# Performance work log

Hardware: AMD Instinct MI355X
Metric: run time of the kernel (lower is better)

The kernel has to match this reference:

```python
import jax, jax.numpy as jnp
import numpy as np

N_ACTOR = 128
NUM_MODS = 6
NUM_PTS = 30
N = 32768
B = 64
EPS = 1e-5


def _gn(x, g, b):
    # torch GroupNorm(1, C) on [..., C]: normalize over channel axis, affine
    m = jnp.mean(x, axis=-1, keepdims=True)
    v = jnp.mean((x - m) ** 2, axis=-1, keepdims=True)
    return (x - m) * jax.lax.rsqrt(v + EPS) * g + b


def setup_inputs() -> dict:
    key = jax.random.key(0)
    ks = jax.random.split(key, 32)
    d = N_ACTOR
    M = NUM_MODS
    s = 0.05
    rn = lambda k, shp: jax.random.normal(k, shp, jnp.float32) * s
    inp = {
        'actors': jax.random.normal(ks[0], (N, d), jnp.float32),
        'actor_ctrs': jax.random.normal(ks[1], (N, 2), jnp.float32),
        'actor_idcs': jnp.arange(N, dtype=jnp.int32).reshape(B, N // B),
        # per-mode residual MLP + output linear (stacked over modes)
        'pred_W1': rn(ks[2], (M, d, d)),
        'pred_g1': jnp.ones((M, d), jnp.float32),
        'pred_b1': jnp.zeros((M, d), jnp.float32),
        'pred_W2': rn(ks[3], (M, d, d)),
        'pred_g2': jnp.ones((M, d), jnp.float32),
        'pred_b2': jnp.zeros((M, d), jnp.float32),
        'pred_Wo': rn(ks[4], (M, d, 2 * NUM_PTS)),
        'pred_bo': rn(ks[5], (M, 2 * NUM_PTS)),
        # cls head: residual MLP + Linear(d,1)
        'cls_W1': rn(ks[6], (d, d)),
        'cls_g1': jnp.ones((d,), jnp.float32),
        'cls_b1': jnp.zeros((d,), jnp.float32),
        'cls_W2': rn(ks[7], (d, d)),
        'cls_g2': jnp.ones((d,), jnp.float32),
        'cls_b2': jnp.zeros((d,), jnp.float32),
        'cls_Wo': rn(ks[8], (d, 1)),
        'cls_bo': rn(ks[9], (1,)),
        # AttDest
        'att_dW1': rn(ks[10], (2, d)),
        'att_db1': rn(ks[11], (d,)),
        'att_dW2': rn(ks[12], (d, d)),
        'att_dg2': jnp.ones((d,), jnp.float32),
        'att_db2': jnp.zeros((d,), jnp.float32),
        'att_aW': rn(ks[13], (2 * d, d)),
        'att_ag': jnp.ones((d,), jnp.float32),
        'att_ab': jnp.zeros((d,), jnp.float32),
    }
    return inp


def reference(actors, actor_ctrs, actor_idcs, pred_W1, pred_g1, pred_b1,
              pred_W2, pred_g2, pred_b2, pred_Wo, pred_bo,
              cls_W1, cls_g1, cls_b1, cls_W2, cls_g2, cls_b2, cls_Wo, cls_bo,
              att_dW1, att_db1, att_dW2, att_dg2, att_db2,
              att_aW, att_ag, att_ab):
    n = actors.shape[0]
    M = pred_W1.shape[0]
    h = jnp.einsum('nc,mcd->mnd', actors, pred_W1)              # [M,N,d]
    h = jax.nn.relu(_gn(h, pred_g1[:, None, :], pred_b1[:, None, :]))
    h = _gn(jnp.einsum('mnd,mde->mne', h, pred_W2),
            pred_g2[:, None, :], pred_b2[:, None, :])
    h = jax.nn.relu(h + actors[None])                           # residual
    preds = jnp.einsum('mnd,mdo->mno', h, pred_Wo) + pred_bo[:, None, :]
    reg = preds.transpose(1, 0, 2).reshape(n, M, NUM_PTS, 2)    # [N,M,T,2]
    # per-scene reg[idcs] += ctrs: actor_idcs partitions arange(N), so this
    # is exactly a per-actor broadcast add of the (concatenated) centers
    reg = reg + actor_ctrs[:, None, None, :]
    dest_ctrs = jax.lax.stop_gradient(reg[:, :, -1, :])         # .detach()
    # --- AttDest ---
    dist = (actor_ctrs[:, None, :] - dest_ctrs).reshape(-1, 2)  # [N*M,2]
    dist = jax.nn.relu(dist @ att_dW1 + att_db1)
    dist = jax.nn.relu(_gn(dist @ att_dW2, att_dg2, att_db2))
    agts = jnp.broadcast_to(actors[:, None, :], (n, M, actors.shape[1]))
    agts = agts.reshape(-1, actors.shape[1])
    feats = jax.nn.relu(_gn(jnp.concatenate([dist, agts], axis=1) @ att_aW,
                            att_ag, att_ab))                    # [N*M,d]
    # --- cls head ---
    c = jax.nn.relu(_gn(feats @ cls_W1, cls_g1, cls_b1))
    c = _gn(c @ cls_W2, cls_g2, cls_b2)
    c = jax.nn.relu(c + feats)
    cls = (c @ cls_Wo + cls_bo).reshape(n, M)
    # --- sort modes by descending score, reorder reg accordingly ---
    order = jnp.argsort(-cls, axis=1)
    cls = jnp.take_along_axis(cls, order, axis=1)
    reg = jnp.take_along_axis(reg, order[:, :, None, None], axis=1)
    # train_model=True concatenates the per-scene splits back in order,
    # which reproduces the full arrays
    return cls, reg
```

## Files before the change

kernel.cpp:

```cpp
#include <hip/hip_runtime.h>

#define EPSV 1e-5f
#define CLS_SZ (32768*6)

#define AL(ch,row) (((ch)<<7) + ((row) ^ ((((ch)&15))<<3)))

__device__ __forceinline__ float4 ld4(const float* p) { return *reinterpret_cast<const float4*>(p); }
__device__ __forceinline__ void st4(float* p, float4 v) { *reinterpret_cast<float4*>(p) = v; }

__device__ __forceinline__ void gemmA(const float* X, const float* __restrict__ Wg,
                                      float* WB0, float* WB1, float (&acc)[8][8],
                                      int ag, int jg4, int tid)
{
  float4 rA = ld4(Wg + tid*4);
  float4 rB = ld4(Wg + 1024 + tid*4);
  __syncthreads();
  st4(WB0 + tid*4, rA);
  st4(WB1 + tid*4, rB);
  __syncthreads();
  #pragma unroll 1
  for (int c = 0; c < 16; ++c) {
    float4 rN;
    const bool pf = (c + 2 < 16);
    if (pf) rN = ld4(Wg + (c+2)*1024 + tid*4);
    const float* WB = (c & 1) ? WB1 : WB0;
    #pragma unroll
    for (int kk = 0; kk < 8; ++kk) {
      int k = c*8 + kk;
      const float* xp = X + (k<<7) + ((ag<<3) ^ ((k & 15)<<3));
      float4 x0 = ld4(xp), x1 = ld4(xp + 4);
      float4 wl = ld4(WB + (kk<<7) + jg4);
      float4 wh = ld4(WB + (kk<<7) + 64 + jg4);
      float xv[8] = {x0.x,x0.y,x0.z,x0.w,x1.x,x1.y,x1.z,x1.w};
      float wv[8] = {wl.x,wl.y,wl.z,wl.w,wh.x,wh.y,wh.z,wh.w};
      #pragma unroll
      for (int r = 0; r < 8; ++r)
        #pragma unroll
        for (int c2 = 0; c2 < 8; ++c2)
          acc[r][c2] = fmaf(xv[r], wv[c2], acc[r][c2]);
    }
    __syncthreads();
    if (pf) st4(((c & 1) ? WB1 : WB0) + tid*4, rN);
  }
}

__device__ __forceinline__ void gemmWo(const float* X, const float* __restrict__ Wg,
                                       float* WB0, float* WB1, float (&acc)[8][4],
                                       int ag, int jg, int tid)
{
  const bool ld = tid < 120;
  const bool zp = (tid >= 120 && tid < 128);
  const int kk0 = ld ? (tid / 15) : (tid - 120);
  const int sl  = ld ? (tid % 15) * 4 : 60;
  float4 rA = {0,0,0,0}, rB = {0,0,0,0};
  if (ld) { rA = ld4(Wg + kk0*60 + sl); rB = ld4(Wg + 480 + kk0*60 + sl); }
  __syncthreads();
  if (ld || zp) { st4(WB0 + (kk0<<6) + sl, rA); st4(WB1 + (kk0<<6) + sl, rB); }
  __syncthreads();
  #pragma unroll 1
  for (int c = 0; c < 16; ++c) {
    float4 rN = {0,0,0,0};
    const bool pf = (c + 2 < 16);
    if (pf && ld) rN = ld4(Wg + (c+2)*480 + kk0*60 + sl);
    const float* WB = (c & 1) ? WB1 : WB0;
    #pragma unroll
    for (int kk = 0; kk < 8; ++kk) {
      int k = c*8 + kk;
      const float* xp = X + (k<<7) + ((ag<<3) ^ ((k & 15)<<3));
      float4 x0 = ld4(xp), x1 = ld4(xp + 4);
      float4 w = ld4(WB + (kk<<6) + jg*4);
      float xv[8] = {x0.x,x0.y,x0.z,x0.w,x1.x,x1.y,x1.z,x1.w};
      float wv[4] = {w.x,w.y,w.z,w.w};
      #pragma unroll
      for (int r = 0; r < 8; ++r)
        #pragma unroll
        for (int c2 = 0; c2 < 4; ++c2)
          acc[r][c2] = fmaf(xv[r], wv[c2], acc[r][c2]);
    }
    __syncthreads();
    if (pf && (ld || zp)) st4(((c & 1) ? WB1 : WB0) + (kk0<<6) + sl, rN);
  }
}

__device__ __forceinline__ void gn_finish(float* PS1, float* PS2, float* MEAN, float* RSTD, int tid)
{
  __syncthreads();
  if (tid < 128) {
    float a = 0.f, b = 0.f;
    #pragma unroll
    for (int j = 0; j < 4; ++j) { a += PS1[tid*4 + j]; b += PS2[tid*4 + j]; }
    float mu = a * 0.0078125f;
    float var = b * 0.0078125f - mu*mu;
    MEAN[tid] = mu;
    RSTD[tid] = rsqrtf(var + EPSV);
  }
  __syncthreads();
}

__device__ __forceinline__ void gn_reduce8(const float (&acc)[8][8], float* PS1, float* PS2,
                                           float* MEAN, float* RSTD, int ag, int jg, int tid)
{
  #pragma unroll
  for (int r = 0; r < 8; ++r) {
    float s = 0.f, q = 0.f;
    #pragma unroll
    for (int c = 0; c < 8; ++c) { float v = acc[r][c]; s += v; q += v*v; }
    s += __shfl_xor(s, 1, 64); q += __shfl_xor(q, 1, 64);
    s += __shfl_xor(s, 2, 64); q += __shfl_xor(q, 2, 64);
    if ((jg & 3) == 0) { int row = ag*8 + r; PS1[row*4 + (jg>>2)] = s; PS2[row*4 + (jg>>2)] = q; }
  }
  gn_finish(PS1, PS2, MEAN, RSTD, tid);
}

__global__ void __launch_bounds__(256, 2) pred_kernel(
    const float* __restrict__ actors, const float* __restrict__ ctrs,
    const float* __restrict__ W1, const float* __restrict__ g1v, const float* __restrict__ b1v,
    const float* __restrict__ W2, const float* __restrict__ g2v, const float* __restrict__ b2v,
    const float* __restrict__ Wo, const float* __restrict__ bov,
    float* __restrict__ out_reg)
{
  __shared__ __align__(16) float ACT[16384];
  __shared__ __align__(16) float WB0[1024], WB1[1024];
  __shared__ float MEAN[128], RSTD[128];
  float* PS1 = WB0;
  float* PS2 = WB1;

  const int tid = threadIdx.x;
  const int jg = tid & 15, ag = tid >> 4;
  const int jg4 = jg*4;
  const int m  = blockIdx.y;
  const int n0 = blockIdx.x * 128;

  #pragma unroll
  for (int p = 0; p < 16; ++p) {
    int i = (p<<8) + tid;
    int r = i >> 5, q4 = (i & 31) << 2;
    float4 v = ld4(actors + (size_t)(n0 + r)*128 + q4);
    ACT[AL(q4+0, r)] = v.x; ACT[AL(q4+1, r)] = v.y;
    ACT[AL(q4+2, r)] = v.z; ACT[AL(q4+3, r)] = v.w;
  }

  float acc[8][8];
  #pragma unroll
  for (int r = 0; r < 8; ++r)
    #pragma unroll
    for (int c = 0; c < 8; ++c) acc[r][c] = 0.f;

  gemmA(ACT, W1 + (size_t)m*16384, WB0, WB1, acc, ag, jg4, tid);
  gn_reduce8(acc, PS1, PS2, MEAN, RSTD, ag, jg, tid);
  {
    float mu[8], rs[8];
    #pragma unroll
    for (int r = 0; r < 8; ++r) { mu[r] = MEAN[ag*8+r]; rs[r] = RSTD[ag*8+r]; }
    float4 gl = ld4(g1v + m*128 + jg4), gh = ld4(g1v + m*128 + 64 + jg4);
    float4 bl = ld4(b1v + m*128 + jg4), bh = ld4(b1v + m*128 + 64 + jg4);
    float gv[8] = {gl.x,gl.y,gl.z,gl.w,gh.x,gh.y,gh.z,gh.w};
    float bv[8] = {bl.x,bl.y,bl.z,bl.w,bh.x,bh.y,bh.z,bh.w};
    float vm[8][8];
    #pragma unroll
    for (int r = 0; r < 8; ++r)
      #pragma unroll
      for (int c = 0; c < 8; ++c)
        vm[r][c] = fmaxf((acc[r][c] - mu[r]) * rs[r] * gv[c] + bv[c], 0.f);
    #pragma unroll
    for (int c = 0; c < 8; ++c) {
      int ch = (c < 4) ? (jg4 + c) : (64 + jg4 + (c - 4));
      int base = (ch<<7) + ((ag<<3) ^ ((ch & 15)<<3));
      st4(ACT + base,     make_float4(vm[0][c],vm[1][c],vm[2][c],vm[3][c]));
      st4(ACT + base + 4, make_float4(vm[4][c],vm[5][c],vm[6][c],vm[7][c]));
    }
  }

  #pragma unroll
  for (int r = 0; r < 8; ++r)
    #pragma unroll
    for (int c = 0; c < 8; ++c) acc[r][c] = 0.f;

  gemmA(ACT, W2 + (size_t)m*16384, WB0, WB1, acc, ag, jg4, tid);
  gn_reduce8(acc, PS1, PS2, MEAN, RSTD, ag, jg, tid);
  {
    float mu[8], rs[8];
    #pragma unroll
    for (int r = 0; r < 8; ++r) { mu[r] = MEAN[ag*8+r]; rs[r] = RSTD[ag*8+r]; }
    float4 gl = ld4(g2v + m*128 + jg4), gh = ld4(g2v + m*128 + 64 + jg4);
    float4 bl = ld4(b2v + m*128 + jg4), bh = ld4(b2v + m*128 + 64 + jg4);
    float gv[8] = {gl.x,gl.y,gl.z,gl.w,gh.x,gh.y,gh.z,gh.w};
    float bv[8] = {bl.x,bl.y,bl.z,bl.w,bh.x,bh.y,bh.z,bh.w};
    float vm[8][8];
    #pragma unroll
    for (int r = 0; r < 8; ++r) {
      const float* ap = actors + (size_t)(n0 + ag*8 + r)*128;
      float4 a0 = ld4(ap + jg4), a1 = ld4(ap + 64 + jg4);
      float av[8] = {a0.x,a0.y,a0.z,a0.w,a1.x,a1.y,a1.z,a1.w};
      #pragma unroll
      for (int c = 0; c < 8; ++c)
        vm[r][c] = fmaxf((acc[r][c] - mu[r]) * rs[r] * gv[c] + bv[c] + av[c], 0.f);
    }
    #pragma unroll
    for (int c = 0; c < 8; ++c) {
      int ch = (c < 4) ? (jg4 + c) : (64 + jg4 + (c - 4));
      int base = (ch<<7) + ((ag<<3) ^ ((ch & 15)<<3));
      st4(ACT + base,     make_float4(vm[0][c],vm[1][c],vm[2][c],vm[3][c]));
      st4(ACT + base + 4, make_float4(vm[4][c],vm[5][c],vm[6][c],vm[7][c]));
    }
  }

  float acc2[8][4];
  #pragma unroll
  for (int r = 0; r < 8; ++r)
    #pragma unroll
    for (int c = 0; c < 4; ++c) acc2[r][c] = 0.f;
  gemmWo(ACT, Wo + (size_t)m*7680, WB0, WB1, acc2, ag, jg, tid);

  if (jg < 15) {
    float4 bo4 = ld4(bov + m*60 + jg4);
    #pragma unroll
    for (int r = 0; r < 8; ++r) {
      int n = n0 + ag*8 + r;
      float2 cc = *reinterpret_cast<const float2*>(ctrs + 2*n);
      float4 v;
      v.x = acc2[r][0] + bo4.x + cc.x;
      v.y = acc2[r][1] + bo4.y + cc.y;
      v.z = acc2[r][2] + bo4.z + cc.x;
      v.w = acc2[r][3] + bo4.w + cc.y;
      st4(out_reg + (size_t)n*360 + m*60 + jg4, v);
    }
  }
}

__global__ void __launch_bounds__(256, 2) att_cls_kernel(
    const float* __restrict__ actors, const float* __restrict__ ctrs,
    const float* __restrict__ dW1, const float* __restrict__ db1,
    const float* __restrict__ dW2, const float* __restrict__ dg2, const float* __restrict__ db2,
    const float* __restrict__ aW, const float* __restrict__ aG, const float* __restrict__ aB,
    const float* __restrict__ cW1, const float* __restrict__ cg1, const float* __restrict__ cb1,
    const float* __restrict__ cW2, const float* __restrict__ cg2, const float* __restrict__ cb2,
    const float* __restrict__ cWo, const float* __restrict__ cbo,
    const float* __restrict__ reg, float* __restrict__ cls_out)
{
  __shared__ __align__(16) float ACT[16384];
  __shared__ __align__(16) float WB0[1024], WB1[1024];
  __shared__ float MEAN[128], RSTD[128];
  float* PS1 = WB0;
  float* PS2 = WB1;
  float* D0x = MEAN;
  float* D0y = RSTD;

  const int tid = threadIdx.x;
  const int jg = tid & 15, ag = tid >> 4;
  const int jg4 = jg*4;
  const int r0 = blockIdx.x * 128;

  if (tid < 128) {
    int rg = r0 + tid;
    int n = rg / 6, mm = rg - 6*n;
    size_t base = (size_t)n*360 + mm*60;
    float2 c2 = *reinterpret_cast<const float2*>(ctrs + 2*n);
    D0x[tid] = c2.x - reg[base + 58];
    D0y[tid] = c2.y - reg[base + 59];
  }
  __syncthreads();

  {
    float dx[8], dy[8];
    #pragma unroll
    for (int r = 0; r < 8; ++r) { dx[r] = D0x[ag*8+r]; dy[r] = D0y[ag*8+r]; }
    #pragma unroll
    for (int c = 0; c < 8; ++c) {
      int ch = (c < 4) ? (jg4 + c) : (64 + jg4 + (c - 4));
      float w1 = dW1[ch], w2 = dW1[128 + ch], bb = db1[ch];
      float v[8];
      #pragma unroll
      for (int r = 0; r < 8; ++r) v[r] = fmaxf(fmaf(dx[r], w1, fmaf(dy[r], w2, bb)), 0.f);
      int base = (ch<<7) + ((ag<<3) ^ ((ch & 15)<<3));
      st4(ACT + base,     make_float4(v[0],v[1],v[2],v[3]));
      st4(ACT + base + 4, make_float4(v[4],v[5],v[6],v[7]));
    }
  }

  float acc[8][8];
  #pragma unroll
  for (int r = 0; r < 8; ++r)
    #pragma unroll
    for (int c = 0; c < 8; ++c) acc[r][c] = 0.f;

  gemmA(ACT, dW2, WB0, WB1, acc, ag, jg4, tid);
  gn_reduce8(acc, PS1, PS2, MEAN, RSTD, ag, jg, tid);
  {
    float mu[8], rs[8];
    #pragma unroll
    for (int r = 0; r < 8; ++r) { mu[r] = MEAN[ag*8+r]; rs[r] = RSTD[ag*8+r]; }
    float4 gl = ld4(dg2 + jg4), gh = ld4(dg2 + 64 + jg4);
    float4 bl = ld4(db2 + jg4), bh = ld4(db2 + 64 + jg4);
    float gv[8] = {gl.x,gl.y,gl.z,gl.w,gh.x,gh.y,gh.z,gh.w};
    float bv[8] = {bl.x,bl.y,bl.z,bl.w,bh.x,bh.y,bh.z,bh.w};
    float vm[8][8];
    #pragma unroll
    for (int r = 0; r < 8; ++r)
      #pragma unroll
      for (int c = 0; c < 8; ++c)
        vm[r][c] = fmaxf((acc[r][c] - mu[r]) * rs[r] * gv[c] + bv[c], 0.f);
    #pragma unroll
    for (int c = 0; c < 8; ++c) {
      int ch = (c < 4) ? (jg4 + c) : (64 + jg4 + (c - 4));
      int base = (ch<<7) + ((ag<<3) ^ ((ch & 15)<<3));
      st4(ACT + base,     make_float4(vm[0][c],vm[1][c],vm[2][c],vm[3][c]));
      st4(ACT + base + 4, make_float4(vm[4][c],vm[5][c],vm[6][c],vm[7][c]));
    }
  }

  #pragma unroll
  for (int r = 0; r < 8; ++r)
    #pragma unroll
    for (int c = 0; c < 8; ++c) acc[r][c] = 0.f;
  gemmA(ACT, aW, WB0, WB1, acc, ag, jg4, tid);
  #pragma unroll
  for (int p = 0; p < 16; ++p) {
    int i = (p<<8) + tid;
    int r = i >> 5, q4 = (i & 31) << 2;
    int n = (r0 + r) / 6;
    float4 v = ld4(actors + (size_t)n*128 + q4);
    ACT[AL(q4+0, r)] = v.x; ACT[AL(q4+1, r)] = v.y;
    ACT[AL(q4+2, r)] = v.z; ACT[AL(q4+3, r)] = v.w;
  }
  gemmA(ACT, aW + 16384, WB0, WB1, acc, ag, jg4, tid);
  gn_reduce8(acc, PS1, PS2, MEAN, RSTD, ag, jg, tid);
  float feats[8][8];
  {
    float mu[8], rs[8];
    #pragma unroll
    for (int r = 0; r < 8; ++r) { mu[r] = MEAN[ag*8+r]; rs[r] = RSTD[ag*8+r]; }
    float4 gl = ld4(aG + jg4), gh = ld4(aG + 64 + jg4);
    float4 bl = ld4(aB + jg4), bh = ld4(aB + 64 + jg4);
    float gv[8] = {gl.x,gl.y,gl.z,gl.w,gh.x,gh.y,gh.z,gh.w};
    float bv[8] = {bl.x,bl.y,bl.z,bl.w,bh.x,bh.y,bh.z,bh.w};
    #pragma unroll
    for (int r = 0; r < 8; ++r)
      #pragma unroll
      for (int c = 0; c < 8; ++c)
        feats[r][c] = fmaxf((acc[r][c] - mu[r]) * rs[r] * gv[c] + bv[c], 0.f);
    #pragma unroll
    for (int c = 0; c < 8; ++c) {
      int ch = (c < 4) ? (jg4 + c) : (64 + jg4 + (c - 4));
      int base = (ch<<7) + ((ag<<3) ^ ((ch & 15)<<3));
      st4(ACT + base,     make_float4(feats[0][c],feats[1][c],feats[2][c],feats[3][c]));
      st4(ACT + base + 4, make_float4(feats[4][c],feats[5][c],feats[6][c],feats[7][c]));
    }
  }

  #pragma unroll
  for (int r = 0; r < 8; ++r)
    #pragma unroll
    for (int c = 0; c < 8; ++c) acc[r][c] = 0.f;
  gemmA(ACT, cW1, WB0, WB1, acc, ag, jg4, tid);
  gn_reduce8(acc, PS1, PS2, MEAN, RSTD, ag, jg, tid);
  {
    float mu[8], rs[8];
    #pragma unroll
    for (int r = 0; r < 8; ++r) { mu[r] = MEAN[ag*8+r]; rs[r] = RSTD[ag*8+r]; }
    float4 gl = ld4(cg1 + jg4), gh = ld4(cg1 + 64 + jg4);
    float4 bl = ld4(cb1 + jg4), bh = ld4(cb1 + 64 + jg4);
    float gv[8] = {gl.x,gl.y,gl.z,gl.w,gh.x,gh.y,gh.z,gh.w};
    float bv[8] = {bl.x,bl.y,bl.z,bl.w,bh.x,bh.y,bh.z,bh.w};
    float vm[8][8];
    #pragma unroll
    for (int r = 0; r < 8; ++r)
      #pragma unroll
      for (int c = 0; c < 8; ++c)
        vm[r][c] = fmaxf((acc[r][c] - mu[r]) * rs[r] * gv[c] + bv[c], 0.f);
    #pragma unroll
    for (int c = 0; c < 8; ++c) {
      int ch = (c < 4) ? (jg4 + c) : (64 + jg4 + (c - 4));
      int base = (ch<<7) + ((ag<<3) ^ ((ch & 15)<<3));
      st4(ACT + base,     make_float4(vm[0][c],vm[1][c],vm[2][c],vm[3][c]));
      st4(ACT + base + 4, make_float4(vm[4][c],vm[5][c],vm[6][c],vm[7][c]));
    }
  }

  #pragma unroll
  for (int r = 0; r < 8; ++r)
    #pragma unroll
    for (int c = 0; c < 8; ++c) acc[r][c] = 0.f;
  gemmA(ACT, cW2, WB0, WB1, acc, ag, jg4, tid);
  gn_reduce8(acc, PS1, PS2, MEAN, RSTD, ag, jg, tid);
  {
    float mu[8], rs[8], p[8];
    #pragma unroll
    for (int r = 0; r < 8; ++r) { mu[r] = MEAN[ag*8+r]; rs[r] = RSTD[ag*8+r]; p[r] = 0.f; }
    float4 gl = ld4(cg2 + jg4), gh = ld4(cg2 + 64 + jg4);
    float4 bl = ld4(cb2 + jg4), bh = ld4(cb2 + 64 + jg4);
    float4 wl = ld4(cWo + jg4), wh = ld4(cWo + 64 + jg4);
    float gv[8] = {gl.x,gl.y,gl.z,gl.w,gh.x,gh.y,gh.z,gh.w};
    float bv[8] = {bl.x,bl.y,bl.z,bl.w,bh.x,bh.y,bh.z,bh.w};
    float wv[8] = {wl.x,wl.y,wl.z,wl.w,wh.x,wh.y,wh.z,wh.w};
    #pragma unroll
    for (int c = 0; c < 8; ++c) {
      #pragma unroll
      for (int r = 0; r < 8; ++r) {
        float v = (acc[r][c] - mu[r]) * rs[r] * gv[c] + bv[c];
        v = fmaxf(v + feats[r][c], 0.f);
        p[r] = fmaf(v, wv[c], p[r]);
      }
    }
    #pragma unroll
    for (int r = 0; r < 8; ++r) {
      float s = p[r];
      s += __shfl_xor(s, 1, 64);
      s += __shfl_xor(s, 2, 64);
      if ((jg & 3) == 0) PS1[(ag*8+r)*4 + (jg>>2)] = s;
    }
  }
  __syncthreads();
  if (tid < 128) {
    float s = 0.f;
    #pragma unroll
    for (int j = 0; j < 4; ++j) s += PS1[tid*4 + j];
    cls_out[r0 + tid] = s + cbo[0];
  }
}

__global__ void __launch_bounds__(256) sort_kernel(float* __restrict__ out)
{
  __shared__ float RL[64*360];
  __shared__ float CL[64*6];
  __shared__ float CS[64*6];
  __shared__ int   ORD[64*6];

  const int tid = threadIdx.x;
  const int n0 = blockIdx.x * 64;
  float* regp = out + CLS_SZ;

  for (int i = tid; i < 64*360; i += 256) RL[i] = regp[(size_t)n0*360 + i];
  for (int i = tid; i < 384; i += 256)    CL[i] = out[n0*6 + i];
  __syncthreads();

  if (tid < 64) {
    float v[6];
    #pragma unroll
    for (int m2 = 0; m2 < 6; ++m2) v[m2] = CL[tid*6 + m2];
    int used = 0;
    for (int j = 0; j < 6; ++j) {
      int best = -1; float bv = 0.f;
      for (int m2 = 0; m2 < 6; ++m2) {
        if (used & (1 << m2)) continue;
        if (best < 0 || v[m2] > bv) { best = m2; bv = v[m2]; }
      }
      used |= (1 << best);
      ORD[tid*6 + j] = best;
      CS[tid*6 + j] = bv;
    }
  }
  __syncthreads();

  for (int i = tid; i < 384; i += 256) out[n0*6 + i] = CS[i];
  for (int i = tid; i < 64*360; i += 256) {
    int rl = i / 360, rem = i - rl*360;
    int slot = rem / 60, j = rem - slot*60;
    out[CLS_SZ + (size_t)n0*360 + i] = RL[rl*360 + ORD[rl*6 + slot]*60 + j];
  }
}

extern "C" void kernel_launch(void* const* d_in, const int* in_sizes, int n_in,
                              void* d_out, int out_size, void* d_ws, size_t ws_size,
                              hipStream_t stream)
{
  (void)in_sizes; (void)n_in; (void)out_size; (void)d_ws; (void)ws_size;
  const float* actors = (const float*)d_in[0];
  const float* ctrs   = (const float*)d_in[1];
  const float* pW1 = (const float*)d_in[3];
  const float* pg1 = (const float*)d_in[4];
  const float* pb1 = (const float*)d_in[5];
  const float* pW2 = (const float*)d_in[6];
  const float* pg2 = (const float*)d_in[7];
  const float* pb2 = (const float*)d_in[8];
  const float* pWo = (const float*)d_in[9];
  const float* pbo = (const float*)d_in[10];
  const float* cW1 = (const float*)d_in[11];
  const float* cg1 = (const float*)d_in[12];
  const float* cb1 = (const float*)d_in[13];
  const float* cW2 = (const float*)d_in[14];
  const float* cg2 = (const float*)d_in[15];
  const float* cb2 = (const float*)d_in[16];
  const float* cWo = (const float*)d_in[17];
  const float* cbo = (const float*)d_in[18];
  const float* dW1 = (const float*)d_in[19];
  const float* db1 = (const float*)d_in[20];
  const float* dW2 = (const float*)d_in[21];
  const float* dg2 = (const float*)d_in[22];
  const float* db2 = (const float*)d_in[23];
  const float* aW  = (const float*)d_in[24];
  const float* aG  = (const float*)d_in[25];
  const float* aB  = (const float*)d_in[26];

  float* out = (float*)d_out;
  float* out_reg = out + CLS_SZ;

  dim3 gA(256, 6);
  pred_kernel<<<gA, 256, 0, stream>>>(actors, ctrs, pW1, pg1, pb1, pW2, pg2, pb2,
                                      pWo, pbo, out_reg);
  att_cls_kernel<<<1536, 256, 0, stream>>>(actors, ctrs,
                                           dW1, db1, dW2, dg2, db2,
                                           aW, aG, aB,
                                           cW1, cg1, cb1, cW2, cg2, cb2, cWo, cbo,
                                           out_reg, out);
  sort_kernel<<<512, 256, 0, stream>>>(out);
}
```

Measured before the change: 753.0 us.

## Split fused attention/cls kernel into two kernels via workspace feats buffer

```diff
diff --git a/kernel.cpp b/kernel.cpp
--- a/kernel.cpp
+++ b/kernel.cpp
@@ -2,6 +2,7 @@
 
 #define EPSV 1e-5f
 #define CLS_SZ (32768*6)
+#define FWS_FLOATS ((size_t)196608 * 128)
 
 #define AL(ch,row) (((ch)<<7) + ((row) ^ ((((ch)&15))<<3)))
 
@@ -228,7 +229,222 @@
   }
 }
 
-__global__ void __launch_bounds__(256, 2) att_cls_kernel(
+__global__ void __launch_bounds__(256, 2) att_feats_kernel(
+    const float* __restrict__ actors, const float* __restrict__ ctrs,
+    const float* __restrict__ dW1, const float* __restrict__ db1,
+    const float* __restrict__ dW2, const float* __restrict__ dg2, const float* __restrict__ db2,
+    const float* __restrict__ aW, const float* __restrict__ aG, const float* __restrict__ aB,
+    const float* __restrict__ reg, float* __restrict__ fws)
+{
+  __shared__ __align__(16) float ACT[16384];
+  __shared__ __align__(16) float WB0[1024], WB1[1024];
+  __shared__ float MEAN[128], RSTD[128];
+  float* PS1 = WB0;
+  float* PS2 = WB1;
+  float* D0x = MEAN;
+  float* D0y = RSTD;
+
+  const int tid = threadIdx.x;
+  const int jg = tid & 15, ag = tid >> 4;
+  const int jg4 = jg*4;
+  const int r0 = blockIdx.x * 128;
+
+  if (tid < 128) {
+    int rg = r0 + tid;
+    int n = rg / 6, mm = rg - 6*n;
+    size_t base = (size_t)n*360 + mm*60;
+    float2 c2 = *reinterpret_cast<const float2*>(ctrs + 2*n);
+    D0x[tid] = c2.x - reg[base + 58];
+    D0y[tid] = c2.y - reg[base + 59];
+  }
+  __syncthreads();
+
+  {
+    float dx[8], dy[8];
+    #pragma unroll
+    for (int r = 0; r < 8; ++r) { dx[r] = D0x[ag*8+r]; dy[r] = D0y[ag*8+r]; }
+    #pragma unroll
+    for (int c = 0; c < 8; ++c) {
+      int ch = (c < 4) ? (jg4 + c) : (64 + jg4 + (c - 4));
+      float w1 = dW1[ch], w2 = dW1[128 + ch], bb = db1[ch];
+      float v[8];
+      #pragma unroll
+      for (int r = 0; r < 8; ++r) v[r] = fmaxf(fmaf(dx[r], w1, fmaf(dy[r], w2, bb)), 0.f);
+      int base = (ch<<7) + ((ag<<3) ^ ((ch & 15)<<3));
+      st4(ACT + base,     make_float4(v[0],v[1],v[2],v[3]));
+      st4(ACT + base + 4, make_float4(v[4],v[5],v[6],v[7]));
+    }
+  }
+
+  float acc[8][8];
+  #pragma unroll
+  for (int r = 0; r < 8; ++r)
+    #pragma unroll
+    for (int c = 0; c < 8; ++c) acc[r][c] = 0.f;
+
+  gemmA(ACT, dW2, WB0, WB1, acc, ag, jg4, tid);
+  gn_reduce8(acc, PS1, PS2, MEAN, RSTD, ag, jg, tid);
+  {
+    float mu[8], rs[8];
+    #pragma unroll
+    for (int r = 0; r < 8; ++r) { mu[r] = MEAN[ag*8+r]; rs[r] = RSTD[ag*8+r]; }
+    float4 gl = ld4(dg2 + jg4), gh = ld4(dg2 + 64 + jg4);
+    float4 bl = ld4(db2 + jg4), bh = ld4(db2 + 64 + jg4);
+    float gv[8] = {gl.x,gl.y,gl.z,gl.w,gh.x,gh.y,gh.z,gh.w};
+    float bv[8] = {bl.x,bl.y,bl.z,bl.w,bh.x,bh.y,bh.z,bh.w};
+    float vm[8][8];
+    #pragma unroll
+    for (int r = 0; r < 8; ++r)
+      #pragma unroll
+      for (int c = 0; c < 8; ++c)
+        vm[r][c] = fmaxf((acc[r][c] - mu[r]) * rs[r] * gv[c] + bv[c], 0.f);
+    #pragma unroll
+    for (int c = 0; c < 8; ++c) {
+      int ch = (c < 4) ? (jg4 + c) : (64 + jg4 + (c - 4));
+      int base = (ch<<7) + ((ag<<3) ^ ((ch & 15)<<3));
+      st4(ACT + base,     make_float4(vm[0][c],vm[1][c],vm[2][c],vm[3][c]));
+      st4(ACT + base + 4, make_float4(vm[4][c],vm[5][c],vm[6][c],vm[7][c]));
+    }
+  }
+
+  #pragma unroll
+  for (int r = 0; r < 8; ++r)
+    #pragma unroll
+    for (int c = 0; c < 8; ++c) acc[r][c] = 0.f;
+  gemmA(ACT, aW, WB0, WB1, acc, ag, jg4, tid);
+  #pragma unroll
+  for (int p = 0; p < 16; ++p) {
+    int i = (p<<8) + tid;
+    int r = i >> 5, q4 = (i & 31) << 2;
+    int n = (r0 + r) / 6;
+    float4 v = ld4(actors + (size_t)n*128 + q4);
+    ACT[AL(q4+0, r)] = v.x; ACT[AL(q4+1, r)] = v.y;
+    ACT[AL(q4+2, r)] = v.z; ACT[AL(q4+3, r)] = v.w;
+  }
+  gemmA(ACT, aW + 16384, WB0, WB1, acc, ag, jg4, tid);
+  gn_reduce8(acc, PS1, PS2, MEAN, RSTD, ag, jg, tid);
+  {
+    float mu[8], rs[8];
+    #pragma unroll
+    for (int r = 0; r < 8; ++r) { mu[r] = MEAN[ag*8+r]; rs[r] = RSTD[ag*8+r]; }
+    float4 gl = ld4(aG + jg4), gh = ld4(aG + 64 + jg4);
+    float4 bl = ld4(aB + jg4), bh = ld4(aB + 64 + jg4);
+    float gv[8] = {gl.x,gl.y,gl.z,gl.w,gh.x,gh.y,gh.z,gh.w};
+    float bv[8] = {bl.x,bl.y,bl.z,bl.w,bh.x,bh.y,bh.z,bh.w};
+    #pragma unroll
+    for (int r = 0; r < 8; ++r) {
+      float fv[8];
+      #pragma unroll
+      for (int c = 0; c < 8; ++c)
+        fv[c] = fmaxf((acc[r][c] - mu[r]) * rs[r] * gv[c] + bv[c], 0.f);
+      float* fp = fws + (size_t)(r0 + ag*8 + r)*128;
+      st4(fp + jg4,      make_float4(fv[0],fv[1],fv[2],fv[3]));
+      st4(fp + 64 + jg4, make_float4(fv[4],fv[5],fv[6],fv[7]));
+    }
+  }
+}
+
+__global__ void __launch_bounds__(256, 2) att_cls2_kernel(
+    const float* __restrict__ cW1, const float* __restrict__ cg1, const float* __restrict__ cb1,
+    const float* __restrict__ cW2, const float* __restrict__ cg2, const float* __restrict__ cb2,
+    const float* __restrict__ cWo, const float* __restrict__ cbo,
+    const float* __restrict__ fws, float* __restrict__ cls_out)
+{
+  __shared__ __align__(16) float ACT[16384];
+  __shared__ __align__(16) float WB0[1024], WB1[1024];
+  __shared__ float MEAN[128], RSTD[128];
+  float* PS1 = WB0;
+  float* PS2 = WB1;
+
+  const int tid = threadIdx.x;
+  const int jg = tid & 15, ag = tid >> 4;
+  const int jg4 = jg*4;
+  const int r0 = blockIdx.x * 128;
+
+  #pragma unroll
+  for (int p = 0; p < 16; ++p) {
+    int i = (p<<8) + tid;
+    int r = i >> 5, q4 = (i & 31) << 2;
+    float4 v = ld4(fws + (size_t)(r0 + r)*128 + q4);
+    ACT[AL(q4+0, r)] = v.x; ACT[AL(q4+1, r)] = v.y;
+    ACT[AL(q4+2, r)] = v.z; ACT[AL(q4+3, r)] = v.w;
+  }
+
+  float acc[8][8];
+  #pragma unroll
+  for (int r = 0; r < 8; ++r)
+    #pragma unroll
+    for (int c = 0; c < 8; ++c) acc[r][c] = 0.f;
+
+  gemmA(ACT, cW1, WB0, WB1, acc, ag, jg4, tid);
+  gn_reduce8(acc, PS1, PS2, MEAN, RSTD, ag, jg, tid);
+  {
+    float mu[8], rs[8];
+    #pragma unroll
+    for (int r = 0; r < 8; ++r) { mu[r] = MEAN[ag*8+r]; rs[r] = RSTD[ag*8+r]; }
+    float4 gl = ld4(cg1 + jg4), gh = ld4(cg1 + 64 + jg4);
+    float4 bl = ld4(cb1 + jg4), bh = ld4(cb1 + 64 + jg4);
+    float gv[8] = {gl.x,gl.y,gl.z,gl.w,gh.x,gh.y,gh.z,gh.w};
+    float bv[8] = {bl.x,bl.y,bl.z,bl.w,bh.x,bh.y,bh.z,bh.w};
+    float vm[8][8];
+    #pragma unroll
+    for (int r = 0; r < 8; ++r)
+      #pragma unroll
+      for (int c = 0; c < 8; ++c)
+        vm[r][c] = fmaxf((acc[r][c] - mu[r]) * rs[r] * gv[c] + bv[c], 0.f);
+    #pragma unroll
+    for (int c = 0; c < 8; ++c) {
+      int ch = (c < 4) ? (jg4 + c) : (64 + jg4 + (c - 4));
+      int base = (ch<<7) + ((ag<<3) ^ ((ch & 15)<<3));
+      st4(ACT + base,     make_float4(vm[0][c],vm[1][c],vm[2][c],vm[3][c]));
+      st4(ACT + base + 4, make_float4(vm[4][c],vm[5][c],vm[6][c],vm[7][c]));
+    }
+  }
+
+  #pragma unroll
+  for (int r = 0; r < 8; ++r)
+    #pragma unroll
+    for (int c = 0; c < 8; ++c) acc[r][c] = 0.f;
+  gemmA(ACT, cW2, WB0, WB1, acc, ag, jg4, tid);
+  gn_reduce8(acc, PS1, PS2, MEAN, RSTD, ag, jg, tid);
+  {
+    float mu[8], rs[8];
+    #pragma unroll
+    for (int r = 0; r < 8; ++r) { mu[r] = MEAN[ag*8+r]; rs[r] = RSTD[ag*8+r]; }
+    float4 gl = ld4(cg2 + jg4), gh = ld4(cg2 + 64 + jg4);
+    float4 bl = ld4(cb2 + jg4), bh = ld4(cb2 + 64 + jg4);
+    float4 wl = ld4(cWo + jg4), wh = ld4(cWo + 64 + jg4);
+    float gv[8] = {gl.x,gl.y,gl.z,gl.w,gh.x,gh.y,gh.z,gh.w};
+    float bv[8] = {bl.x,bl.y,bl.z,bl.w,bh.x,bh.y,bh.z,bh.w};
+    float wv[8] = {wl.x,wl.y,wl.z,wl.w,wh.x,wh.y,wh.z,wh.w};
+    #pragma unroll
+    for (int r = 0; r < 8; ++r) {
+      const float* fp = fws + (size_t)(r0 + ag*8 + r)*128;
+      float4 a0 = ld4(fp + jg4), a1 = ld4(fp + 64 + jg4);
+      float av[8] = {a0.x,a0.y,a0.z,a0.w,a1.x,a1.y,a1.z,a1.w};
+      float p = 0.f;
+      #pragma unroll
+      for (int c = 0; c < 8; ++c) {
+        float v = (acc[r][c] - mu[r]) * rs[r] * gv[c] + bv[c];
+        v = fmaxf(v + av[c], 0.f);
+        p = fmaf(v, wv[c], p);
+      }
+      float s = p;
+      s += __shfl_xor(s, 1, 64);
+      s += __shfl_xor(s, 2, 64);
+      if ((jg & 3) == 0) PS1[(ag*8+r)*4 + (jg>>2)] = s;
+    }
+  }
+  __syncthreads();
+  if (tid < 128) {
+    float s = 0.f;
+    #pragma unroll
+    for (int j = 0; j < 4; ++j) s += PS1[tid*4 + j];
+    cls_out[r0 + tid] = s + cbo[0];
+  }
+}
+
+__global__ void __launch_bounds__(256, 2) att_cls_mono_kernel(
     const float* __restrict__ actors, const float* __restrict__ ctrs,
     const float* __restrict__ dW1, const float* __restrict__ db1,
     const float* __restrict__ dW2, const float* __restrict__ dg2, const float* __restrict__ db2,
@@ -464,7 +680,7 @@
                               void* d_out, int out_size, void* d_ws, size_t ws_size,
                               hipStream_t stream)
 {
-  (void)in_sizes; (void)n_in; (void)out_size; (void)d_ws; (void)ws_size;
+  (void)in_sizes; (void)n_in; (void)out_size;
   const float* actors = (const float*)d_in[0];
   const float* ctrs   = (const float*)d_in[1];
   const float* pW1 = (const float*)d_in[3];
@@ -494,14 +710,24 @@
 
   float* out = (float*)d_out;
   float* out_reg = out + CLS_SZ;
+  float* fws = (float*)d_ws;
+  const bool split = ws_size >= FWS_FLOATS * sizeof(float);
 
   dim3 gA(256, 6);
   pred_kernel<<<gA, 256, 0, stream>>>(actors, ctrs, pW1, pg1, pb1, pW2, pg2, pb2,
                                       pWo, pbo, out_reg);
-  att_cls_kernel<<<1536, 256, 0, stream>>>(actors, ctrs,
-                                           dW1, db1, dW2, dg2, db2,
-                                           aW, aG, aB,
-                                           cW1, cg1, cb1, cW2, cg2, cb2, cWo, cbo,
-                                           out_reg, out);
+  if (split) {
+    att_feats_kernel<<<1536, 256, 0, stream>>>(actors, ctrs,
+                                               dW1, db1, dW2, dg2, db2,
+                                               aW, aG, aB, out_reg, fws);
+    att_cls2_kernel<<<1536, 256, 0, stream>>>(cW1, cg1, cb1, cW2, cg2, cb2,
+                                              cWo, cbo, fws, out);
+  } else {
+    att_cls_mono_kernel<<<1536, 256, 0, stream>>>(actors, ctrs,
+                                                  dW1, db1, dW2, dg2, db2,
+                                                  aW, aG, aB,
+                                                  cW1, cg1, cb1, cW2, cg2, cb2, cWo, cbo,
+                                                  out_reg, out);
+  }
   sort_kernel<<<512, 256, 0, stream>>>(out);
 }
```

Result: no change. 767.9 us (+2.0%).
